# Kernel optimization log

Hardware: AMD Instinct MI355X
Metric: run time of the kernel (lower is better)

Reference implementation:

```python
import jax, jax.numpy as jnp
import numpy as np

IN_DIM, BANDS = 42, 22
H_VAD, H_NOISE, H_DEN = 24, 48, 96


def gru(x, w_ih, w_hh, b_ih, b_hh):
    """torch.nn.GRU (batch_first) semantics, h0=0.
    x: [B,T,D]; w_ih: [3H,D]; w_hh: [3H,H]; gate order r,z,n."""
    H = w_hh.shape[1]
    # precompute input projections for all timesteps (big GEMM, recurrence only on H)
    xp = jnp.einsum('btd,gd->btg', x, w_ih) + b_ih  # [B,T,3H]

    def step(h, xt):
        hp = h @ w_hh.T + b_hh
        xr, xz, xn = jnp.split(xt, 3, axis=-1)
        hr, hz, hn = jnp.split(hp, 3, axis=-1)
        r = jax.nn.sigmoid(xr + hr)
        z = jax.nn.sigmoid(xz + hz)
        n = jnp.tanh(xn + r * hn)
        h_new = (1.0 - z) * n + z * h
        return h_new, h_new

    h0 = jnp.zeros((x.shape[0], H), x.dtype)
    _, hs = jax.lax.scan(step, h0, jnp.swapaxes(xp, 0, 1))  # [T,B,H]
    return jnp.swapaxes(hs, 0, 1)  # [B,T,H]


def setup_inputs() -> dict:
    key = jax.random.key(0)
    ks = jax.random.split(key, 20)

    def w(k, shape, fan):
        return (jax.random.normal(k, shape, jnp.float32) / np.sqrt(fan)).astype(jnp.float32)

    B, T = 256, 2000
    d_noise_in = H_VAD + H_VAD + IN_DIM     # 90
    d_den_in = H_VAD + H_NOISE + IN_DIM     # 114
    return {
        'x': jax.random.normal(ks[0], (B, T, IN_DIM), jnp.float32),
        'in_w': w(ks[1], (H_VAD, IN_DIM), IN_DIM),
        'in_b': jnp.zeros((H_VAD,), jnp.float32),
        'vad_wih': w(ks[2], (3 * H_VAD, H_VAD), H_VAD),
        'vad_whh': w(ks[3], (3 * H_VAD, H_VAD), H_VAD),
        'vad_bih': jnp.zeros((3 * H_VAD,), jnp.float32),
        'vad_bhh': jnp.zeros((3 * H_VAD,), jnp.float32),
        'vad_out_w': w(ks[4], (1, H_VAD), H_VAD),
        'vad_out_b': jnp.zeros((1,), jnp.float32),
        'noise_wih': w(ks[5], (3 * H_NOISE, d_noise_in), d_noise_in),
        'noise_whh': w(ks[6], (3 * H_NOISE, H_NOISE), H_NOISE),
        'noise_bih': jnp.zeros((3 * H_NOISE,), jnp.float32),
        'noise_bhh': jnp.zeros((3 * H_NOISE,), jnp.float32),
        'den_wih': w(ks[7], (3 * H_DEN, d_den_in), d_den_in),
        'den_whh': w(ks[8], (3 * H_DEN, H_DEN), H_DEN),
        'den_bih': jnp.zeros((3 * H_DEN,), jnp.float32),
        'den_bhh': jnp.zeros((3 * H_DEN,), jnp.float32),
        'out_w': w(ks[9], (BANDS, H_DEN), H_DEN),
        'out_b': jnp.zeros((BANDS,), jnp.float32),
    }


def reference(x, in_w, in_b, vad_wih, vad_whh, vad_bih, vad_bhh,
              vad_out_w, vad_out_b, noise_wih, noise_whh, noise_bih, noise_bhh,
              den_wih, den_whh, den_bih, den_bhh, out_w, out_b):
    tmp = jnp.tanh(jnp.einsum('btd,hd->bth', x, in_w) + in_b)          # [B,T,24]
    vad_h = gru(tmp, vad_wih, vad_whh, vad_bih, vad_bhh)               # [B,T,24]
    vad = jax.nn.sigmoid(jnp.einsum('bth,oh->bto', vad_h, vad_out_w) + vad_out_b)
    noise_in = jnp.concatenate([tmp, vad_h, x], axis=-1)               # [B,T,90]
    noise_h = gru(noise_in, noise_wih, noise_whh, noise_bih, noise_bhh)  # [B,T,48]
    den_in = jnp.concatenate([vad_h, noise_h, x], axis=-1)             # [B,T,114]
    den_h = gru(den_in, den_wih, den_whh, den_bih, den_bhh)            # [B,T,96]
    gains = jax.nn.sigmoid(jnp.einsum('bth,oh->bto', den_h, out_w) + out_b)
    return gains, vad
```

## Files before the change

### kernel.cpp

```cpp
#include <hip/hip_runtime.h>

typedef _Float16 f16;
typedef _Float16 h2 __attribute__((ext_vector_type(2)));
typedef unsigned int u32;

#define TB  256
#define TTT 2000
#define INW 42
#define HV  24
#define HN  48
#define HD  96
#define NTH 640

#define DIN 0
#define DH  128
#define NIN 224
#define NH  320
#define ACTW 384

__device__ __forceinline__ float fsigm(float v) {
    return __builtin_amdgcn_rcpf(1.0f + __builtin_amdgcn_exp2f(-1.44269504089f * v));
}
__device__ __forceinline__ float ftanh(float v) {
    float e = __builtin_amdgcn_exp2f(2.88539008178f * v);
    return 1.0f - 2.0f * __builtin_amdgcn_rcpf(e + 1.0f);
}
__device__ __forceinline__ float dot2f(u32 a, u32 w, float c) {
#if __has_builtin(__builtin_amdgcn_fdot2)
    return __builtin_amdgcn_fdot2(__builtin_bit_cast(h2, a), __builtin_bit_cast(h2, w), c, false);
#else
    h2 av = __builtin_bit_cast(h2, a), wv = __builtin_bit_cast(h2, w);
    return c + (float)av[0] * (float)wv[0] + (float)av[1] * (float)wv[1];
#endif
}
__device__ __forceinline__ u32 packw(float a, float b) {
    h2 v; v[0] = (f16)a; v[1] = (f16)b;
    return __builtin_bit_cast(u32, v);
}
template<int CTRL>
__device__ __forceinline__ float dpp_add(float x) {
    int y = __builtin_amdgcn_mov_dpp(__builtin_bit_cast(int, x), CTRL, 0xF, 0xF, true);
    return x + __builtin_bit_cast(float, y);
}
template<int CTRL, int RMASK>
__device__ __forceinline__ float dpp_add_m(float x) {
    int y = __builtin_amdgcn_update_dpp(0, __builtin_bit_cast(int, x), CTRL, RMASK, 0xF, false);
    return x + __builtin_bit_cast(float, y);
}

#define SYNCB() asm volatile("s_waitcnt lgkmcnt(0)\n\ts_barrier" ::: "memory")

#define ACCI(AV, W, IDX) do { u32 _a = (AV); \
    rr = dot2f(_a, W[0][IDX], rr); zz = dot2f(_a, W[1][IDX], zz); an = dot2f(_a, W[2][IDX], an); } while (0)
#define ACCH(AV, W, IDX) do { u32 _a = (AV); \
    rr = dot2f(_a, W[0][IDX], rr); zz = dot2f(_a, W[1][IDX], zz); hn = dot2f(_a, W[2][IDX], hn); } while (0)
#define ACCI4(U4, W, M0) do { uint4 _u4 = (U4); \
    ACCI(_u4.x, W, (M0)+0); ACCI(_u4.y, W, (M0)+1); ACCI(_u4.z, W, (M0)+2); ACCI(_u4.w, W, (M0)+3); } while (0)
#define ACCH4(U4, W, M0) do { uint4 _u4 = (U4); \
    ACCH(_u4.x, W, (M0)+0); ACCH(_u4.y, W, (M0)+1); ACCH(_u4.z, W, (M0)+2); ACCH(_u4.w, W, (M0)+3); } while (0)
#define RED4_Q() do { \
    rr = dpp_add<0xB1>(rr); rr = dpp_add<0x4E>(rr); \
    zz = dpp_add<0xB1>(zz); zz = dpp_add<0x4E>(zz); \
    an = dpp_add<0xB1>(an); an = dpp_add<0x4E>(an); \
    hn = dpp_add<0xB1>(hn); hn = dpp_add<0x4E>(hn); } while (0)
#define RED4_1() do { \
    rr = dpp_add<0xB1>(rr); zz = dpp_add<0xB1>(zz); \
    an = dpp_add<0xB1>(an); hn = dpp_add<0xB1>(hn); } while (0)

template<int N> struct IC { static constexpr int val = N; };

__global__ __launch_bounds__(NTH, 1) void rnnoise_kernel(
    const float* __restrict__ gx,
    const float* __restrict__ in_w,      const float* __restrict__ in_b,
    const float* __restrict__ vad_wih,   const float* __restrict__ vad_whh,
    const float* __restrict__ vad_bih,   const float* __restrict__ vad_bhh,
    const float* __restrict__ vad_out_w, const float* __restrict__ vad_out_b,
    const float* __restrict__ noise_wih, const float* __restrict__ noise_whh,
    const float* __restrict__ noise_bih, const float* __restrict__ noise_bhh,
    const float* __restrict__ den_wih,   const float* __restrict__ den_whh,
    const float* __restrict__ den_bih,   const float* __restrict__ den_bhh,
    const float* __restrict__ out_w,     const float* __restrict__ out_b,
    float* __restrict__ gains, float* __restrict__ vout)
{
    __shared__ __align__(16) f16 act[8][ACTW];

    const int tid = threadIdx.x, wid = tid >> 6, lane = tid & 63;
    const int b = blockIdx.x;

    #pragma unroll
    for (int i = 0; i < 3; ++i) {
        int idx = tid + i * NTH;
        if (idx < 8 * ACTW / 2) ((u32*)act)[idx] = 0u;
    }
    __syncthreads();

    const int role = (wid == 8) ? 2 : ((wid == 4 || wid == 5 || wid == 9) ? 1 : 0);

    if (role == 0) {
        const int dwi = (wid < 4) ? wid : (wid - 2);
        const int u = 16 * dwi + (lane >> 2), q = lane & 3;
        const bool ow = (wid == 6 || wid == 7);
        const int o = ((wid == 7) ? 11 : 0) + (lane >> 2);
        const int oc = (ow && o < 22) ? o : 0;
        const bool ostore = (ow && (lane & 3) == 0 && o < 22);
        u32 wdi[3][16], wdh[3][12], wo[12];
        #pragma unroll
        for (int g = 0; g < 3; ++g) {
            const float* wi = den_wih + (g * HD + u) * 114;
            #pragma unroll
            for (int m = 0; m < 16; ++m) {
                int c = 32 * q + 2 * m;
                float a  = (c     < 114) ? wi[c]     : 0.f;
                float b2 = (c + 1 < 114) ? wi[c + 1] : 0.f;
                wdi[g][m] = packw(a, b2);
            }
            const float* wh = den_whh + (g * HD + u) * HD + 24 * q;
            #pragma unroll
            for (int m = 0; m < 12; ++m) wdh[g][m] = packw(wh[2*m], wh[2*m+1]);
        }
        #pragma unroll
        for (int m = 0; m < 12; ++m)
            wo[m] = ow ? packw(out_w[oc*HD + 24*q + 2*m], out_w[oc*HD + 24*q + 2*m + 1]) : 0u;
        const float bdr  = den_bih[u]        + den_bhh[u];
        const float bdz  = den_bih[HD + u]   + den_bhh[HD + u];
        const float bdni = den_bih[2*HD + u];
        const float bdnh = den_bhh[2*HD + u];
        const float bo   = ow ? out_b[oc] : 0.f;
        float hreg = 0.f;
        uint4 a0{}, a1{}, a2{}, a3{};

        auto step = [&](auto PC, auto GC, int k) {
            constexpr int P = decltype(PC)::val;
            constexpr bool G = decltype(GC)::val != 0;
            constexpr int SHH = (P + 2) & 7;
            constexpr int SWR = (P + 3) & 7;
            constexpr int SNX = (P + 4) & 7;
            const uint4* hp = (const uint4*)&act[SHH][DH + 24 * q];
            uint4 h0 = hp[0], h1 = hp[1], h2 = hp[2];
            float rr = 0, zz = 0, an = 0, hn = 0;
            ACCI4(a0, wdi, 0); ACCI4(a1, wdi, 4); ACCI4(a2, wdi, 8); ACCI4(a3, wdi, 12);
            {
                const uint4* ip = (const uint4*)&act[SNX][DIN + 32 * q];
                a0 = ip[0]; a1 = ip[1]; a2 = ip[2]; a3 = ip[3];
            }
            ACCH4(h0, wdh, 0); ACCH4(h1, wdh, 4); ACCH4(h2, wdh, 8);
            RED4_Q();
            if (!G || (k >= 5 && k < TTT + 5)) {
                float r = fsigm(rr + bdr);
                float z = fsigm(zz + bdz);
                float n = ftanh(an + bdni + r * (hn + bdnh));
                hreg = z * (hreg - n) + n;
                if (q == 0) act[SWR][DH + u] = (f16)hreg;
            }
            if (ow && (!G || (k >= 6 && k < TTT + 6))) {
                float acc = 0;
                acc = dot2f(h0.x, wo[0], acc);  acc = dot2f(h0.y, wo[1], acc);
                acc = dot2f(h0.z, wo[2], acc);  acc = dot2f(h0.w, wo[3], acc);
                acc = dot2f(h1.x, wo[4], acc);  acc = dot2f(h1.y, wo[5], acc);
                acc = dot2f(h1.z, wo[6], acc);  acc = dot2f(h1.w, wo[7], acc);
                acc = dot2f(h2.x, wo[8], acc);  acc = dot2f(h2.y, wo[9], acc);
                acc = dot2f(h2.z, wo[10], acc); acc = dot2f(h2.w, wo[11], acc);
                acc = dpp_add<0xB1>(acc); acc = dpp_add<0x4E>(acc);
                if (ostore)
                    gains[((size_t)b * TTT + (k - 6)) * 22 + o] = fsigm(acc + bo);
            }
            SYNCB();
        };
        auto block8 = [&](auto GC, int k0) {
            step(IC<0>{},GC,k0);   step(IC<1>{},GC,k0+1); step(IC<2>{},GC,k0+2); step(IC<3>{},GC,k0+3);
            step(IC<4>{},GC,k0+4); step(IC<5>{},GC,k0+5); step(IC<6>{},GC,k0+6); step(IC<7>{},GC,k0+7);
        };
        #pragma clang loop unroll(disable)
        for (int k0 = 0; k0 < 16; k0 += 8) block8(IC<1>{}, k0);
        #pragma clang loop unroll(disable)
        for (int k0 = 16; k0 < TTT - 16; k0 += 8) block8(IC<0>{}, k0);
        #pragma clang loop unroll(disable)
        for (int k0 = TTT - 16; k0 < TTT + 8; k0 += 8) block8(IC<1>{}, k0);

    } else if (role == 1) {
        const int nwi = (wid == 4) ? 0 : ((wid == 5) ? 1 : 2);
        const int u = 16 * nwi + (lane >> 2), q = lane & 3;
        u32 wni[3][12], wnh[3][8];
        #pragma unroll
        for (int g = 0; g < 3; ++g) {
            const float* wi = noise_wih + (g * HN + u) * 90;
            #pragma unroll
            for (int m = 0; m < 12; ++m) {
                int c = 24 * q + 2 * m;
                float a  = (c     < 90) ? wi[c]     : 0.f;
                float b2 = (c + 1 < 90) ? wi[c + 1] : 0.f;
                wni[g][m] = packw(a, b2);
            }
            const float* wh = noise_whh + (g * HN + u) * HN;
            #pragma unroll
            for (int m = 0; m < 8; ++m) {
                int c = 16 * q + 2 * m;
                float a  = (c     < 48) ? wh[c]     : 0.f;
                float b2 = (c + 1 < 48) ? wh[c + 1] : 0.f;
                wnh[g][m] = packw(a, b2);
            }
        }
        const float bnr  = noise_bih[u]        + noise_bhh[u];
        const float bnz  = noise_bih[HN + u]   + noise_bhh[HN + u];
        const float bnni = noise_bih[2*HN + u];
        const float bnnh = noise_bhh[2*HN + u];
        float hreg = 0.f;
        uint4 a0{}, a1{}, a2{};

        auto step = [&](auto PC, auto GC, int k) {
            constexpr int P = decltype(PC)::val;
            constexpr bool G = decltype(GC)::val != 0;
            constexpr int SHH = (P + 4) & 7;
            constexpr int SWR = (P + 5) & 7;
            constexpr int SNX = (P + 6) & 7;
            const uint4* hp = (const uint4*)&act[SHH][NH + 16 * q];
            uint4 h0 = hp[0], h1 = hp[1];
            float rr = 0, zz = 0, an = 0, hn = 0;
            ACCI4(a0, wni, 0); ACCI4(a1, wni, 4); ACCI4(a2, wni, 8);
            {
                const uint4* ip = (const uint4*)&act[SNX][NIN + 24 * q];
                a0 = ip[0]; a1 = ip[1]; a2 = ip[2];
            }
            ACCH4(h0, wnh, 0); ACCH4(h1, wnh, 4);
            RED4_Q();
            if (!G || (k >= 3 && k < TTT + 3)) {
                float r = fsigm(rr + bnr);
                float z = fsigm(zz + bnz);
                float n = ftanh(an + bnni + r * (hn + bnnh));
                hreg = z * (hreg - n) + n;
                if (q == 0) {
                    f16 hh = (f16)hreg;
                    act[SWR][NH + u]       = hh;
                    act[SWR][DIN + 24 + u] = hh;
                }
            }
            SYNCB();
        };
        auto block8 = [&](auto GC, int k0) {
            step(IC<0>{},GC,k0);   step(IC<1>{},GC,k0+1); step(IC<2>{},GC,k0+2); step(IC<3>{},GC,k0+3);
            step(IC<4>{},GC,k0+4); step(IC<5>{},GC,k0+5); step(IC<6>{},GC,k0+6); step(IC<7>{},GC,k0+7);
        };
        #pragma clang loop unroll(disable)
        for (int k0 = 0; k0 < 16; k0 += 8) block8(IC<1>{}, k0);
        #pragma clang loop unroll(disable)
        for (int k0 = 16; k0 < TTT - 16; k0 += 8) block8(IC<0>{}, k0);
        #pragma clang loop unroll(disable)
        for (int k0 = TTT - 16; k0 < TTT + 8; k0 += 8) block8(IC<1>{}, k0);

    } else {
        const int l = lane;
        const int u = (l < 48) ? (l >> 1) : 0, q2 = l & 1;
        u32 wvi[3][6], wvh[3][6], wtm[12];
        float bvr = 0, bvz = 0, bvni = 0, bvnh = 0, btm = 0, wvo_u = 0;
        if (l < 48) {
            #pragma unroll
            for (int g = 0; g < 3; ++g) {
                const float* wi = vad_wih + (g * HV + u) * HV + 12 * q2;
                const float* wh = vad_whh + (g * HV + u) * HV + 12 * q2;
                #pragma unroll
                for (int j = 0; j < 6; ++j) {
                    wvi[g][j] = packw(wi[2*j], wi[2*j+1]);
                    wvh[g][j] = packw(wh[2*j], wh[2*j+1]);
                }
            }
            #pragma unroll
            for (int j = 0; j < 12; ++j) {
                int c0 = 24 * q2 + 2 * j;
                float a = (c0     < INW) ? in_w[u * INW + c0]     : 0.f;
                float c = (c0 + 1 < INW) ? in_w[u * INW + c0 + 1] : 0.f;
                wtm[j] = packw(a, c);
            }
            bvr  = vad_bih[u]        + vad_bhh[u];
            bvz  = vad_bih[HV + u]   + vad_bhh[HV + u];
            bvni = vad_bih[2*HV + u];
            bvnh = vad_bhh[2*HV + u];
            btm  = in_b[u];
            if (q2 == 0) wvo_u = vad_out_w[u];
        }
        const float bvo = vad_out_b[0];
        float hreg = 0.f;

        float xa = 0, xb = 0, xc = 0, xd = 0;
        if (l < INW) {
            float x0v = gx[((size_t)b * TTT + 0) * INW + l];
            xb = gx[((size_t)b * TTT + 1) * INW + l];
            xc = gx[((size_t)b * TTT + 2) * INW + l];
            xd = gx[((size_t)b * TTT + 3) * INW + l];
            xa = gx[((size_t)b * TTT + 4) * INW + l];
            f16 xh = (f16)x0v;
            act[0][NIN + 48 + l] = xh;
            act[0][DIN + 72 + l] = xh;
        }

        auto step = [&](auto PC, auto GC, int k) {
            constexpr int P = decltype(PC)::val;
            constexpr bool G = decltype(GC)::val != 0;
            constexpr int SX = (P + 1) & 7;
            constexpr int ST = (P + 7) & 7;
            constexpr int SH = (P + 6) & 7;
            constexpr int XR = (P + 1) & 3;
            const uint2* tp = (const uint2*)&act[ST][NIN + 12 * q2];
            uint2 t0 = tp[0], t1 = tp[1], t2 = tp[2];
            const uint2* hp = (const uint2*)&act[SH][NIN + 24 + 12 * q2];
            uint2 g0 = hp[0], g1 = hp[1], g2 = hp[2];
            const uint4* xp = (const uint4*)&act[P][NIN + 48 + 24 * q2];
            uint4 xv0 = xp[0], xv1 = xp[1], xv2 = xp[2];
            if ((!G || k + 1 < TTT) && l < INW) {
                float xv;
                if constexpr (XR == 0) xv = xa; else if constexpr (XR == 1) xv = xb;
                else if constexpr (XR == 2) xv = xc; else xv = xd;
                f16 xh = (f16)xv;
                act[SX][NIN + 48 + l] = xh;
                act[SX][DIN + 72 + l] = xh;
            }
            if ((!G || k + 5 < TTT) && l < INW) {
                float xv = gx[((size_t)b * TTT + (k + 5)) * INW + l];
                if constexpr (XR == 0) xa = xv; else if constexpr (XR == 1) xb = xv;
                else if constexpr (XR == 2) xc = xv; else xd = xv;
            }
            if (!G || (k >= 1 && k <= TTT)) {
                float rr = 0, zz = 0, an = 0, hn = 0;
                ACCI(t0.x, wvi, 0); ACCI(t0.y, wvi, 1);
                ACCH(g0.x, wvh, 0); ACCH(g0.y, wvh, 1);
                ACCI(t1.x, wvi, 2); ACCI(t1.y, wvi, 3);
                ACCH(g1.x, wvh, 2); ACCH(g1.y, wvh, 3);
                ACCI(t2.x, wvi, 4); ACCI(t2.y, wvi, 5);
                ACCH(g2.x, wvh, 4); ACCH(g2.y, wvh, 5);
                RED4_1();
                float r = fsigm(rr + bvr);
                float z = fsigm(zz + bvz);
                float n = ftanh(an + bvni + r * (hn + bvnh));
                hreg = z * (hreg - n) + n;
                if (l < 48 && q2 == 0) {
                    f16 hh = (f16)hreg;
                    act[ST][NIN + 24 + u] = hh;
                    act[ST][DIN + u]      = hh;
                }
                float val = (l < 48 && q2 == 0) ? (wvo_u * hreg) : 0.f;
                val = dpp_add<0xB1>(val);  val = dpp_add<0x4E>(val);
                val = dpp_add<0x124>(val); val = dpp_add<0x128>(val);
                val = dpp_add_m<0x142, 0xA>(val);
                val = dpp_add_m<0x143, 0xC>(val);
                if (l == 63) vout[(size_t)b * TTT + (k - 1)] = fsigm(val + bvo);
            }
            if (!G || k < TTT) {
                float acc = 0;
                acc = dot2f(xv0.x, wtm[0], acc);  acc = dot2f(xv0.y, wtm[1], acc);
                acc = dot2f(xv0.z, wtm[2], acc);  acc = dot2f(xv0.w, wtm[3], acc);
                acc = dot2f(xv1.x, wtm[4], acc);  acc = dot2f(xv1.y, wtm[5], acc);
                acc = dot2f(xv1.z, wtm[6], acc);  acc = dot2f(xv1.w, wtm[7], acc);
                acc = dot2f(xv2.x, wtm[8], acc);  acc = dot2f(xv2.y, wtm[9], acc);
                acc = dot2f(xv2.z, wtm[10], acc); acc = dot2f(xv2.w, wtm[11], acc);
                acc = dpp_add<0xB1>(acc);
                if (l < 48 && q2 == 0) act[P][NIN + u] = (f16)ftanh(acc + btm);
            }
            SYNCB();
        };
        auto block8 = [&](auto GC, int k0) {
            step(IC<0>{},GC,k0);   step(IC<1>{},GC,k0+1); step(IC<2>{},GC,k0+2); step(IC<3>{},GC,k0+3);
            step(IC<4>{},GC,k0+4); step(IC<5>{},GC,k0+5); step(IC<6>{},GC,k0+6); step(IC<7>{},GC,k0+7);
        };
        #pragma clang loop unroll(disable)
        for (int k0 = 0; k0 < 16; k0 += 8) block8(IC<1>{}, k0);
        #pragma clang loop unroll(disable)
        for (int k0 = 16; k0 < TTT - 16; k0 += 8) block8(IC<0>{}, k0);
        #pragma clang loop unroll(disable)
        for (int k0 = TTT - 16; k0 < TTT + 8; k0 += 8) block8(IC<1>{}, k0);
    }
}

extern "C" void kernel_launch(void* const* d_in, const int* in_sizes, int n_in,
                              void* d_out, int out_size, void* d_ws, size_t ws_size,
                              hipStream_t stream) {
    (void)in_sizes; (void)n_in; (void)d_ws; (void)ws_size; (void)out_size;
    const float* gx        = (const float*)d_in[0];
    const float* in_w      = (const float*)d_in[1];
    const float* in_b      = (const float*)d_in[2];
    const float* vad_wih   = (const float*)d_in[3];
    const float* vad_whh   = (const float*)d_in[4];
    const float* vad_bih   = (const float*)d_in[5];
    const float* vad_bhh   = (const float*)d_in[6];
    const float* vad_out_w = (const float*)d_in[7];
    const float* vad_out_b = (const float*)d_in[8];
    const float* noise_wih = (const float*)d_in[9];
    const float* noise_whh = (const float*)d_in[10];
    const float* noise_bih = (const float*)d_in[11];
    const float* noise_bhh = (const float*)d_in[12];
    const float* den_wih   = (const float*)d_in[13];
    const float* den_whh   = (const float*)d_in[14];
    const float* den_bih   = (const float*)d_in[15];
    const float* den_bhh   = (const float*)d_in[16];
    const float* out_w     = (const float*)d_in[17];
    const float* out_b     = (const float*)d_in[18];
    float* gains = (float*)d_out;
    float* vout  = (float*)d_out + (size_t)TB * (size_t)TTT * 22;

    rnnoise_kernel<<<dim3(TB), dim3(NTH), 0, stream>>>(
        gx, in_w, in_b, vad_wih, vad_whh, vad_bih, vad_bhh, vad_out_w, vad_out_b,
        noise_wih, noise_whh, noise_bih, noise_bhh, den_wih, den_whh, den_bih, den_bhh,
        out_w, out_b, gains, vout);
}
```

Before: 1.582 ms.

## Split denoise GRU reduction across 8 lanes with 16 waves per block

Raises the block from 10 to 16 waves and gives the denoise GRU 12 waves. Each hidden unit's dot products are now split over 8 lanes instead of 4, so every lane does half as many dot2 operations per step and holds fewer weight registers. A third DPP step finishes the reduction. The LDS activation layout is widened and the noise/VAD wave ids are remapped. The cost is more waves taking part in every per-step barrier and an extra DPP reduction level on the serial recurrence path.

```diff
diff --git a/kernel.cpp b/kernel.cpp
--- a/kernel.cpp
+++ b/kernel.cpp
@@ -10,13 +10,13 @@
 #define HV  24
 #define HN  48
 #define HD  96
-#define NTH 640
+#define NTH 1024
 
 #define DIN 0
 #define DH  128
-#define NIN 224
-#define NH  320
-#define ACTW 384
+#define NIN 256
+#define NH  352
+#define ACTW 416
 
 __device__ __forceinline__ float fsigm(float v) {
     return __builtin_amdgcn_rcpf(1.0f + __builtin_amdgcn_exp2f(-1.44269504089f * v));
@@ -63,6 +63,11 @@
     zz = dpp_add<0xB1>(zz); zz = dpp_add<0x4E>(zz); \
     an = dpp_add<0xB1>(an); an = dpp_add<0x4E>(an); \
     hn = dpp_add<0xB1>(hn); hn = dpp_add<0x4E>(hn); } while (0)
+#define RED8_T() do { \
+    rr = dpp_add<0xB1>(rr); rr = dpp_add<0x4E>(rr); rr = dpp_add<0x124>(rr); \
+    zz = dpp_add<0xB1>(zz); zz = dpp_add<0x4E>(zz); zz = dpp_add<0x124>(zz); \
+    an = dpp_add<0xB1>(an); an = dpp_add<0x4E>(an); an = dpp_add<0x124>(an); \
+    hn = dpp_add<0xB1>(hn); hn = dpp_add<0x4E>(hn); hn = dpp_add<0x124>(hn); } while (0)
 #define RED4_1() do { \
     rr = dpp_add<0xB1>(rr); zz = dpp_add<0xB1>(zz); \
     an = dpp_add<0xB1>(an); hn = dpp_add<0xB1>(hn); } while (0)
@@ -87,47 +92,53 @@
     const int tid = threadIdx.x, wid = tid >> 6, lane = tid & 63;
     const int b = blockIdx.x;
 
-    #pragma unroll
-    for (int i = 0; i < 3; ++i) {
-        int idx = tid + i * NTH;
+    {
+        int idx = tid;
+        if (idx < 8 * ACTW / 2) ((u32*)act)[idx] = 0u;
+        idx = tid + NTH;
         if (idx < 8 * ACTW / 2) ((u32*)act)[idx] = 0u;
     }
     __syncthreads();
 
-    const int role = (wid == 8) ? 2 : ((wid == 4 || wid == 5 || wid == 9) ? 1 : 0);
+    const int role = (wid == 15) ? 2 : ((wid >= 12) ? 1 : 0);
 
     if (role == 0) {
-        const int dwi = (wid < 4) ? wid : (wid - 2);
-        const int u = 16 * dwi + (lane >> 2), q = lane & 3;
-        const bool ow = (wid == 6 || wid == 7);
-        const int o = ((wid == 7) ? 11 : 0) + (lane >> 2);
-        const int oc = (ow && o < 22) ? o : 0;
-        const bool ostore = (ow && (lane & 3) == 0 && o < 22);
-        u32 wdi[3][16], wdh[3][12], wo[12];
+        const int r8 = lane & 7;
+        const int u  = 8 * wid + (lane >> 3);
+        const bool ow = (wid < 3);
+        const int o  = 8 * wid + (lane >> 3);
+        const int oc = (o < 22) ? o : 0;
+        const bool tlane  = ((lane & 7) == 4);
+        u32 wdi[3][8], wdh[3][8], wo[8];
         #pragma unroll
         for (int g = 0; g < 3; ++g) {
             const float* wi = den_wih + (g * HD + u) * 114;
+            const float* wh = den_whh + (g * HD + u) * HD;
             #pragma unroll
-            for (int m = 0; m < 16; ++m) {
-                int c = 32 * q + 2 * m;
+            for (int m = 0; m < 8; ++m) {
+                int c = 16 * r8 + 2 * m;
                 float a  = (c     < 114) ? wi[c]     : 0.f;
                 float b2 = (c + 1 < 114) ? wi[c + 1] : 0.f;
                 wdi[g][m] = packw(a, b2);
-            }
-            const float* wh = den_whh + (g * HD + u) * HD + 24 * q;
-            #pragma unroll
-            for (int m = 0; m < 12; ++m) wdh[g][m] = packw(wh[2*m], wh[2*m+1]);
+                float ha  = (c     < 96) ? wh[c]     : 0.f;
+                float hb  = (c + 1 < 96) ? wh[c + 1] : 0.f;
+                wdh[g][m] = packw(ha, hb);
+            }
         }
         #pragma unroll
-        for (int m = 0; m < 12; ++m)
-            wo[m] = ow ? packw(out_w[oc*HD + 24*q + 2*m], out_w[oc*HD + 24*q + 2*m + 1]) : 0u;
+        for (int m = 0; m < 8; ++m) {
+            int c = 16 * r8 + 2 * m;
+            float a  = (ow && c     < 96) ? out_w[oc * HD + c]     : 0.f;
+            float b2 = (ow && c + 1 < 96) ? out_w[oc * HD + c + 1] : 0.f;
+            wo[m] = packw(a, b2);
+        }
         const float bdr  = den_bih[u]        + den_bhh[u];
         const float bdz  = den_bih[HD + u]   + den_bhh[HD + u];
         const float bdni = den_bih[2*HD + u];
         const float bdnh = den_bhh[2*HD + u];
         const float bo   = ow ? out_b[oc] : 0.f;
         float hreg = 0.f;
-        uint4 a0{}, a1{}, a2{}, a3{};
+        uint4 a0{}, a1{};
 
         auto step = [&](auto PC, auto GC, int k) {
             constexpr int P = decltype(PC)::val;
@@ -135,33 +146,31 @@
             constexpr int SHH = (P + 2) & 7;
             constexpr int SWR = (P + 3) & 7;
             constexpr int SNX = (P + 4) & 7;
-            const uint4* hp = (const uint4*)&act[SHH][DH + 24 * q];
-            uint4 h0 = hp[0], h1 = hp[1], h2 = hp[2];
+            const uint4* hp = (const uint4*)&act[SHH][DH + 16 * r8];
+            uint4 h0 = hp[0], h1 = hp[1];
             float rr = 0, zz = 0, an = 0, hn = 0;
-            ACCI4(a0, wdi, 0); ACCI4(a1, wdi, 4); ACCI4(a2, wdi, 8); ACCI4(a3, wdi, 12);
+            ACCI4(a0, wdi, 0); ACCI4(a1, wdi, 4);
             {
-                const uint4* ip = (const uint4*)&act[SNX][DIN + 32 * q];
-                a0 = ip[0]; a1 = ip[1]; a2 = ip[2]; a3 = ip[3];
-            }
-            ACCH4(h0, wdh, 0); ACCH4(h1, wdh, 4); ACCH4(h2, wdh, 8);
-            RED4_Q();
+                const uint4* ip = (const uint4*)&act[SNX][DIN + 16 * r8];
+                a0 = ip[0]; a1 = ip[1];
+            }
+            ACCH4(h0, wdh, 0); ACCH4(h1, wdh, 4);
+            RED8_T();
             if (!G || (k >= 5 && k < TTT + 5)) {
                 float r = fsigm(rr + bdr);
                 float z = fsigm(zz + bdz);
                 float n = ftanh(an + bdni + r * (hn + bdnh));
                 hreg = z * (hreg - n) + n;
-                if (q == 0) act[SWR][DH + u] = (f16)hreg;
+                if (tlane) act[SWR][DH + u] = (f16)hreg;
             }
             if (ow && (!G || (k >= 6 && k < TTT + 6))) {
                 float acc = 0;
-                acc = dot2f(h0.x, wo[0], acc);  acc = dot2f(h0.y, wo[1], acc);
-                acc = dot2f(h0.z, wo[2], acc);  acc = dot2f(h0.w, wo[3], acc);
-                acc = dot2f(h1.x, wo[4], acc);  acc = dot2f(h1.y, wo[5], acc);
-                acc = dot2f(h1.z, wo[6], acc);  acc = dot2f(h1.w, wo[7], acc);
-                acc = dot2f(h2.x, wo[8], acc);  acc = dot2f(h2.y, wo[9], acc);
-                acc = dot2f(h2.z, wo[10], acc); acc = dot2f(h2.w, wo[11], acc);
-                acc = dpp_add<0xB1>(acc); acc = dpp_add<0x4E>(acc);
-                if (ostore)
+                acc = dot2f(h0.x, wo[0], acc); acc = dot2f(h0.y, wo[1], acc);
+                acc = dot2f(h0.z, wo[2], acc); acc = dot2f(h0.w, wo[3], acc);
+                acc = dot2f(h1.x, wo[4], acc); acc = dot2f(h1.y, wo[5], acc);
+                acc = dot2f(h1.z, wo[6], acc); acc = dot2f(h1.w, wo[7], acc);
+                acc = dpp_add<0xB1>(acc); acc = dpp_add<0x4E>(acc); acc = dpp_add<0x124>(acc);
+                if (tlane && o < 22)
                     gains[((size_t)b * TTT + (k - 6)) * 22 + o] = fsigm(acc + bo);
             }
             SYNCB();
@@ -178,7 +187,7 @@
         for (int k0 = TTT - 16; k0 < TTT + 8; k0 += 8) block8(IC<1>{}, k0);
 
     } else if (role == 1) {
-        const int nwi = (wid == 4) ? 0 : ((wid == 5) ? 1 : 2);
+        const int nwi = wid - 12;
         const int u = 16 * nwi + (lane >> 2), q = lane & 3;
         u32 wni[3][12], wnh[3][8];
         #pragma unroll
```

Measured after the change: 1.763 ms. 1.11x slower.
